# Optimization experiments

Measured on AMD Instinct MI355X. Metric: run time of the kernel, lower is better.

Reference implementation:

```python
import jax, jax.numpy as jnp
import numpy as np

B, T, C, H = 8192, 16, 256, 4
HS = C // H  # 64
FF = 4 * C   # 1024
EPS = 1e-5


def layer_norm(x, g, b):
    mu = jnp.mean(x, axis=-1, keepdims=True)
    var = jnp.var(x, axis=-1, keepdims=True)
    return (x - mu) / jnp.sqrt(var + EPS) * g + b


def setup_inputs() -> dict:
    key = jax.random.key(0)
    ks = jax.random.split(key, 12)
    s = C ** -0.5
    return {
        "x": jax.random.normal(ks[0], (B, T, C), dtype=jnp.float32),
        "Wq": jax.random.normal(ks[1], (H, C, HS), dtype=jnp.float32) * s,
        "Wk": jax.random.normal(ks[2], (H, C, HS), dtype=jnp.float32) * s,
        "Wv": jax.random.normal(ks[3], (H, C, HS), dtype=jnp.float32) * s,
        "Wo": jax.random.normal(ks[4], (C, C), dtype=jnp.float32) * s,
        "bo": jnp.zeros((C,), dtype=jnp.float32),
        "W1": jax.random.normal(ks[5], (C, FF), dtype=jnp.float32) * s,
        "b1": jnp.zeros((FF,), dtype=jnp.float32),
        "W2": jax.random.normal(ks[6], (FF, C), dtype=jnp.float32) * (FF ** -0.5),
        "b2": jnp.zeros((C,), dtype=jnp.float32),
        "g1": jnp.ones((C,), dtype=jnp.float32),
        "be1": jnp.zeros((C,), dtype=jnp.float32),
        "g2": jnp.ones((C,), dtype=jnp.float32),
        "be2": jnp.zeros((C,), dtype=jnp.float32),
    }


def reference(x, Wq, Wk, Wv, Wo, bo, W1, b1, W2, b2, g1, be1, g2, be2):
    # pre-LN attention
    h = layer_norm(x, g1, be1)                       # [B,T,C]
    q = jnp.einsum('btc,hcd->bhtd', h, Wq)
    k = jnp.einsum('btc,hcd->bhtd', h, Wk)
    v = jnp.einsum('btc,hcd->bhtd', h, Wv)
    # NOTE: original scales by n_embed**-0.5 (C), not head_size**-0.5
    scores = jnp.einsum('bhtd,bhsd->bhts', q, k) * (C ** -0.5)
    causal = jnp.tril(jnp.ones((T, T), dtype=bool))
    scores = jnp.where(causal, scores, -jnp.inf)
    w = jax.nn.softmax(scores, axis=-1)
    attn = jnp.einsum('bhts,bhsd->bhtd', w, v)       # [B,H,T,HS]
    attn = attn.transpose(0, 2, 1, 3).reshape(B, T, C)
    x = x + attn @ Wo + bo
    # pre-LN MLP
    h2 = layer_norm(x, g2, be2)
    x = x + jax.nn.relu(h2 @ W1 + b1) @ W2 + b2
    return x
```

## Files before the change

### kernel.cpp

```cpp
#include <hip/hip_runtime.h>
#include <stdint.h>
#include <stddef.h>


#define NTH 512

using f32x4 = __attribute__((ext_vector_type(4))) float;
using s16x8 = __attribute__((ext_vector_type(8))) short;

__device__ __forceinline__ uint16_t f2bf(float f) {
  union { float f; uint32_t u; } v; v.f = f;
  uint32_t r = v.u + 0x7FFF + ((v.u >> 16) & 1);
  return (uint16_t)(r >> 16);
}

__global__ void cvt_qkv(const float* __restrict__ Wq, const float* __restrict__ Wk,
                        const float* __restrict__ Wv, uint16_t* __restrict__ dst) {
  int tid = blockIdx.x * 256 + threadIdx.x;
  if (tid >= 4 * 192 * 256) return;
  int h = tid / (192 * 256);
  int r = tid % (192 * 256);
  int n = r / 256, k = r % 256;
  int comp = n >> 6, d = n & 63;
  const float* src = (comp == 0) ? Wq : ((comp == 1) ? Wk : Wv);
  dst[tid] = f2bf(src[(size_t)h * 256 * 64 + (size_t)k * 64 + d]);
}

__global__ void cvt_t(const float* __restrict__ W, uint16_t* __restrict__ dst,
                      int K, int N) {
  int tid = blockIdx.x * 256 + threadIdx.x;
  if (tid >= K * N) return;
  int n = tid / K, k = tid % K;
  dst[tid] = f2bf(W[(size_t)k * N + n]);
}

#define OFF_H     0
#define OFF_STG   67584
#define OFF_SCR   88064
#define OFF_Q     (OFF_SCR + 0)
#define OFF_K     (OFF_SCR + 18432)
#define OFF_VT    (OFF_SCR + 36864)
#define OFF_P     (OFF_SCR + 61440)
#define OFF_STATS (OFF_SCR + 61440)
#define OFF_U     (OFF_SCR + 0)
#define LDS_BYTES 159744

__device__ __forceinline__ void stageB(const uint16_t* __restrict__ src, int strideK,
                                       int kk0, int nrows, char* stg, int tid) {
  int chunks = nrows * 4;
  for (int idx = tid; idx < chunks; idx += NTH) {
    int n = idx >> 2, o = idx & 3;
    uint4 v = *(const uint4*)(src + (size_t)n * strideK + kk0 + o * 8);
    *(uint4*)(stg + n * 80 + o * 16) = v;
  }
}

__global__ __launch_bounds__(NTH, 2) void block_fused(
    const float* __restrict__ xg,
    const uint16_t* __restrict__ qkvt, const uint16_t* __restrict__ wot,
    const uint16_t* __restrict__ w1t, const uint16_t* __restrict__ w2t,
    const float* __restrict__ bo, const float* __restrict__ b1,
    const float* __restrict__ b2, const float* __restrict__ g1,
    const float* __restrict__ be1, const float* __restrict__ g2,
    const float* __restrict__ be2, float* __restrict__ outg) {
  __shared__ __align__(16) char lds[LDS_BYTES];
  const int tid = threadIdx.x;
  const int wave = tid >> 6, lane = tid & 63;
  const int quad = lane >> 4, l15 = lane & 15;
  const int wr = wave >> 2, wc = wave & 3;
  const int row0 = blockIdx.x * 128;

  {
    uint32_t* z = (uint32_t*)(lds + OFF_VT);
    for (int i = tid; i < (24576 + 10240) / 4; i += NTH) z[i] = 0;
  }

  {
    const int r = tid >> 2;
    const int seg = tid & 3;
    const float* xrow = xg + (size_t)(row0 + r) * 256 + seg * 64;
    float s = 0.f, sq = 0.f;
#pragma unroll
    for (int i = 0; i < 16; ++i) {
      float4 v = ((const float4*)xrow)[i];
      s += v.x + v.y + v.z + v.w;
      sq += v.x * v.x + v.y * v.y + v.z * v.z + v.w * v.w;
    }
    s += __shfl_xor(s, 1); s += __shfl_xor(s, 2);
    sq += __shfl_xor(sq, 1); sq += __shfl_xor(sq, 2);
    float mu = s * (1.f / 256.f);
    float var = sq * (1.f / 256.f) - mu * mu;
    float rstd = rsqrtf(var + 1e-5f);
    char* hrow = lds + OFF_H + r * 528 + seg * 128;
    const float* g1p = g1 + seg * 64;
    const float* e1p = be1 + seg * 64;
#pragma unroll
    for (int i = 0; i < 16; ++i) {
      float4 v = ((const float4*)xrow)[i];
      float4 gv = ((const float4*)g1p)[i];
      float4 bv = ((const float4*)e1p)[i];
      uint32_t p0 = (uint32_t)f2bf((v.x - mu) * rstd * gv.x + bv.x) |
                    ((uint32_t)f2bf((v.y - mu) * rstd * gv.y + bv.y) << 16);
      uint32_t p1 = (uint32_t)f2bf((v.z - mu) * rstd * gv.z + bv.z) |
                    ((uint32_t)f2bf((v.w - mu) * rstd * gv.w + bv.w) << 16);
      uint2 u; u.x = p0; u.y = p1;
      *(uint2*)(hrow + i * 8) = u;
    }
  }
  __syncthreads();

  const f32x4 zero4 = {0.f, 0.f, 0.f, 0.f};
  f32x4 yacc[4][4];
#pragma unroll
  for (int mt = 0; mt < 4; ++mt)
#pragma unroll
    for (int nt = 0; nt < 4; ++nt) yacc[mt][nt] = zero4;

  for (int h = 0; h < 4; ++h) {
    f32x4 qa[4][3];
#pragma unroll
    for (int mt = 0; mt < 4; ++mt)
#pragma unroll
      for (int nt = 0; nt < 3; ++nt) qa[mt][nt] = zero4;
    const uint16_t* wsrc = qkvt + (size_t)h * 192 * 256;
    for (int ks = 0; ks < 8; ++ks) {
      stageB(wsrc, 256, ks * 32, 192, lds + OFF_STG, tid);
      __syncthreads();
      s16x8 af[4], bf[3];
#pragma unroll
      for (int mt = 0; mt < 4; ++mt)
        af[mt] = *(const s16x8*)(lds + OFF_H + (64 * wr + 16 * mt + l15) * 528 +
                                 (ks * 32 + quad * 8) * 2);
#pragma unroll
      for (int nt = 0; nt < 3; ++nt)
        bf[nt] = *(const s16x8*)(lds + OFF_STG + (48 * wc + 16 * nt + l15) * 80 +
                                 quad * 16);
#pragma unroll
      for (int mt = 0; mt < 4; ++mt)
#pragma unroll
        for (int nt = 0; nt < 3; ++nt)
          qa[mt][nt] = __builtin_amdgcn_mfma_f32_16x16x32_bf16(af[mt], bf[nt],
                                                               qa[mt][nt], 0, 0, 0);
      __syncthreads();
    }
#pragma unroll
    for (int mt = 0; mt < 4; ++mt) {
#pragma unroll
      for (int nt = 0; nt < 3; ++nt) {
        int col = 48 * wc + 16 * nt + l15;
        int comp = col >> 6, d = col & 63;
#pragma unroll
        for (int reg = 0; reg < 4; ++reg) {
          int grow = 64 * wr + 16 * mt + 4 * quad + reg;
          uint16_t v = f2bf(qa[mt][nt][reg]);
          if (comp == 0)
            *(uint16_t*)(lds + OFF_Q + grow * 144 + d * 2) = v;
          else if (comp == 1)
            *(uint16_t*)(lds + OFF_K + grow * 144 + d * 2) = v;
          else
            *(uint16_t*)(lds + OFF_VT + (grow >> 4) * 3072 + d * 48 +
                         (grow & 15) * 2) = v;
        }
      }
    }
    __syncthreads();

    {
      f32x4 sacc = zero4;
#pragma unroll
      for (int kk = 0; kk < 2; ++kk) {
        s16x8 aq = *(const s16x8*)(lds + OFF_Q + (16 * wave + l15) * 144 +
                                   (kk * 32 + quad * 8) * 2);
        s16x8 bk = *(const s16x8*)(lds + OFF_K + (16 * wave + l15) * 144 +
                                   (kk * 32 + quad * 8) * 2);
        sacc = __builtin_amdgcn_mfma_f32_16x16x32_bf16(aq, bk, sacc, 0, 0, 0);
      }
      char* pb = lds + OFF_P + wave * 1280;
#pragma unroll
      for (int reg = 0; reg < 4; ++reg) {
        int t = 4 * quad + reg, ss = l15;
        float sc = sacc[reg] * 0.0625f;
        if (ss > t) sc = -1e30f;
        float mx = sc;
#pragma unroll
        for (int d = 1; d < 16; d <<= 1) mx = fmaxf(mx, __shfl_xor(mx, d, 16));
        float e = __expf(sc - mx);
        float sm = e;
#pragma unroll
        for (int d = 1; d < 16; d <<= 1) sm += __shfl_xor(sm, d, 16);
        *(uint16_t*)(pb + t * 80 + ss * 2) = f2bf(e / sm);
      }
      s16x8 ap = *(const s16x8*)(pb + l15 * 80 + quad * 16);
      f32x4 oacc[4];
#pragma unroll
      for (int nt = 0; nt < 4; ++nt) {
        s16x8 bv = *(const s16x8*)(lds + OFF_VT + wave * 3072 +
                                   (16 * nt + l15) * 48 + quad * 16);
        oacc[nt] = __builtin_amdgcn_mfma_f32_16x16x32_bf16(ap, bv, zero4, 0, 0, 0);
      }
#pragma unroll
      for (int nt = 0; nt < 4; ++nt)
#pragma unroll
        for (int reg = 0; reg < 4; ++reg)
          *(uint16_t*)(lds + OFF_Q + (16 * wave + 4 * quad + reg) * 144 +
                       (16 * nt + l15) * 2) = f2bf(oacc[nt][reg]);
    }
    __syncthreads();

    for (int ks = 0; ks < 2; ++ks) {
      stageB(wot, 256, h * 64 + ks * 32, 256, lds + OFF_STG, tid);
      __syncthreads();
      s16x8 af[4], bf[4];
#pragma unroll
      for (int mt = 0; mt < 4; ++mt)
        af[mt] = *(const s16x8*)(lds + OFF_Q + (64 * wr + 16 * mt + l15) * 144 +
                                 (ks * 32 + quad * 8) * 2);
#pragma unroll
      for (int nt = 0; nt < 4; ++nt)
        bf[nt] = *(const s16x8*)(lds + OFF_STG + (64 * wc + 16 * nt + l15) * 80 +
                                 quad * 16);
#pragma unroll
      for (int mt = 0; mt < 4; ++mt)
#pragma unroll
        for (int nt = 0; nt < 4; ++nt)
          yacc[mt][nt] = __builtin_amdgcn_mfma_f32_16x16x32_bf16(af[mt], bf[nt],
                                                                 yacc[mt][nt], 0, 0, 0);
      __syncthreads();
    }
  }

#pragma unroll
  for (int nt = 0; nt < 4; ++nt) {
    int col = 64 * wc + 16 * nt + l15;
    float bov = bo[col];
#pragma unroll
    for (int mt = 0; mt < 4; ++mt)
#pragma unroll
      for (int reg = 0; reg < 4; ++reg) {
        int grow = row0 + 64 * wr + 16 * mt + 4 * quad + reg;
        yacc[mt][nt][reg] += xg[(size_t)grow * 256 + col] + bov;
      }
  }

  {
    float* stats = (float*)(lds + OFF_STATS);
#pragma unroll
    for (int mt = 0; mt < 4; ++mt)
#pragma unroll
      for (int reg = 0; reg < 4; ++reg) {
        float ps = 0.f, pq = 0.f;
#pragma unroll
        for (int nt = 0; nt < 4; ++nt) {
          float v = yacc[mt][nt][reg];
          ps += v; pq += v * v;
        }
#pragma unroll
        for (int d = 1; d < 16; d <<= 1) {
          ps += __shfl_xor(ps, d, 16);
          pq += __shfl_xor(pq, d, 16);
        }
        if (l15 == 0) {
          int lrow = 64 * wr + 16 * mt + 4 * quad + reg;
          stats[lrow * 8 + wc] = ps;
          stats[lrow * 8 + 4 + wc] = pq;
        }
      }
    __syncthreads();
    float g2v[4], e2v[4];
#pragma unroll
    for (int nt = 0; nt < 4; ++nt) {
      int col = 64 * wc + 16 * nt + l15;
      g2v[nt] = g2[col]; e2v[nt] = be2[col];
    }
#pragma unroll
    for (int mt = 0; mt < 4; ++mt)
#pragma unroll
      for (int reg = 0; reg < 4; ++reg) {
        int lrow = 64 * wr + 16 * mt + 4 * quad + reg;
        f32x4 s0 = *(const f32x4*)(stats + lrow * 8);
        f32x4 s1 = *(const f32x4*)(stats + lrow * 8 + 4);
        float mu = (s0[0] + s0[1] + s0[2] + s0[3]) * (1.f / 256.f);
        float var = (s1[0] + s1[1] + s1[2] + s1[3]) * (1.f / 256.f) - mu * mu;
        float rstd = rsqrtf(var + 1e-5f);
#pragma unroll
        for (int nt = 0; nt < 4; ++nt) {
          float hv = (yacc[mt][nt][reg] - mu) * rstd * g2v[nt] + e2v[nt];
          *(uint16_t*)(lds + OFF_H + lrow * 528 + (64 * wc + 16 * nt + l15) * 2) =
              f2bf(hv);
        }
      }
    __syncthreads();
  }

#pragma unroll
  for (int nt = 0; nt < 4; ++nt) {
    float b2v = b2[64 * wc + 16 * nt + l15];
#pragma unroll
    for (int mt = 0; mt < 4; ++mt)
#pragma unroll
      for (int reg = 0; reg < 4; ++reg) yacc[mt][nt][reg] += b2v;
  }
  for (int fc = 0; fc < 4; ++fc) {
    f32x4 ua[4][4];
#pragma unroll
    for (int mt = 0; mt < 4; ++mt)
#pragma unroll
      for (int nt = 0; nt < 4; ++nt) ua[mt][nt] = zero4;
    const uint16_t* w1src = w1t + (size_t)(fc * 256) * 256;
    for (int ks = 0; ks < 8; ++ks) {
      stageB(w1src, 256, ks * 32, 256, lds + OFF_STG, tid);
      __syncthreads();
      s16x8 af[4], bf[4];
#pragma unroll
      for (int mt = 0; mt < 4; ++mt)
        af[mt] = *(const s16x8*)(lds + OFF_H + (64 * wr + 16 * mt + l15) * 528 +
                                 (ks * 32 + quad * 8) * 2);
#pragma unroll
      for (int nt = 0; nt < 4; ++nt)
        bf[nt] = *(const s16x8*)(lds + OFF_STG + (64 * wc + 16 * nt + l15) * 80 +
                                 quad * 16);
#pragma unroll
      for (int mt = 0; mt < 4; ++mt)
#pragma unroll
        for (int nt = 0; nt < 4; ++nt)
          ua[mt][nt] = __builtin_amdgcn_mfma_f32_16x16x32_bf16(af[mt], bf[nt],
                                                               ua[mt][nt], 0, 0, 0);
      __syncthreads();
    }
#pragma unroll
    for (int nt = 0; nt < 4; ++nt) {
      float b1v = b1[fc * 256 + 64 * wc + 16 * nt + l15];
#pragma unroll
      for (int mt = 0; mt < 4; ++mt)
#pragma unroll
        for (int reg = 0; reg < 4; ++reg) {
          float uv = fmaxf(ua[mt][nt][reg] + b1v, 0.f);
          *(uint16_t*)(lds + OFF_U + (64 * wr + 16 * mt + 4 * quad + reg) * 528 +
                       (64 * wc + 16 * nt + l15) * 2) = f2bf(uv);
        }
    }
    __syncthreads();
    for (int ks = 0; ks < 8; ++ks) {
      stageB(w2t, 1024, fc * 256 + ks * 32, 256, lds + OFF_STG, tid);
      __syncthreads();
      s16x8 af[4], bf[4];
#pragma unroll
      for (int mt = 0; mt < 4; ++mt)
        af[mt] = *(const s16x8*)(lds + OFF_U + (64 * wr + 16 * mt + l15) * 528 +
                                 (ks * 32 + quad * 8) * 2);
#pragma unroll
      for (int nt = 0; nt < 4; ++nt)
        bf[nt] = *(const s16x8*)(lds + OFF_STG + (64 * wc + 16 * nt + l15) * 80 +
                                 quad * 16);
#pragma unroll
      for (int mt = 0; mt < 4; ++mt)
#pragma unroll
        for (int nt = 0; nt < 4; ++nt)
          yacc[mt][nt] = __builtin_amdgcn_mfma_f32_16x16x32_bf16(af[mt], bf[nt],
                                                                 yacc[mt][nt], 0, 0, 0);
      __syncthreads();
    }
  }

#pragma unroll
  for (int mt = 0; mt < 4; ++mt)
#pragma unroll
    for (int nt = 0; nt < 4; ++nt) {
      int col = 64 * wc + 16 * nt + l15;
#pragma unroll
      for (int reg = 0; reg < 4; ++reg) {
        int grow = row0 + 64 * wr + 16 * mt + 4 * quad + reg;
        outg[(size_t)grow * 256 + col] = yacc[mt][nt][reg];
      }
    }
}

extern "C" void kernel_launch(void* const* d_in, const int* in_sizes, int n_in,
                              void* d_out, int out_size, void* d_ws, size_t ws_size,
                              hipStream_t stream) {
  (void)in_sizes; (void)n_in; (void)out_size; (void)ws_size;
  const float* x   = (const float*)d_in[0];
  const float* Wq  = (const float*)d_in[1];
  const float* Wk  = (const float*)d_in[2];
  const float* Wv  = (const float*)d_in[3];
  const float* Wo  = (const float*)d_in[4];
  const float* bo  = (const float*)d_in[5];
  const float* W1  = (const float*)d_in[6];
  const float* b1  = (const float*)d_in[7];
  const float* W2  = (const float*)d_in[8];
  const float* b2  = (const float*)d_in[9];
  const float* g1  = (const float*)d_in[10];
  const float* be1 = (const float*)d_in[11];
  const float* g2  = (const float*)d_in[12];
  const float* be2 = (const float*)d_in[13];

  uint16_t* ws   = (uint16_t*)d_ws;
  uint16_t* qkvt = ws;
  uint16_t* wot  = ws + 196608;
  uint16_t* w1t  = ws + 262144;
  uint16_t* w2t  = ws + 524288;

  cvt_qkv<<<768, 256, 0, stream>>>(Wq, Wk, Wv, qkvt);
  cvt_t<<<256, 256, 0, stream>>>(Wo, wot, 256, 256);
  cvt_t<<<1024, 256, 0, stream>>>(W1, w1t, 256, 1024);
  cvt_t<<<1024, 256, 0, stream>>>(W2, w2t, 1024, 256);

  block_fused<<<1024, NTH, 0, stream>>>(x, qkvt, wot, w1t, w2t, bo, b1, b2, g1,
                                        be1, g2, be2, (float*)d_out);
}
```

Measured before the change: 748.5 us.

## Register-prefetch weight tiles in GEMM phases and merge weight conversion kernels

```diff
diff --git a/kernel.cpp b/kernel.cpp
--- a/kernel.cpp
+++ b/kernel.cpp
@@ -14,24 +14,39 @@
   return (uint16_t)(r >> 16);
 }
 
-__global__ void cvt_qkv(const float* __restrict__ Wq, const float* __restrict__ Wk,
-                        const float* __restrict__ Wv, uint16_t* __restrict__ dst) {
-  int tid = blockIdx.x * 256 + threadIdx.x;
-  if (tid >= 4 * 192 * 256) return;
-  int h = tid / (192 * 256);
-  int r = tid % (192 * 256);
-  int n = r / 256, k = r % 256;
-  int comp = n >> 6, d = n & 63;
-  const float* src = (comp == 0) ? Wq : ((comp == 1) ? Wk : Wv);
-  dst[tid] = f2bf(src[(size_t)h * 256 * 64 + (size_t)k * 64 + d]);
-}
-
-__global__ void cvt_t(const float* __restrict__ W, uint16_t* __restrict__ dst,
-                      int K, int N) {
-  int tid = blockIdx.x * 256 + threadIdx.x;
-  if (tid >= K * N) return;
-  int n = tid / K, k = tid % K;
-  dst[tid] = f2bf(W[(size_t)k * N + n]);
+__global__ void cvt_all(const float* __restrict__ Wq, const float* __restrict__ Wk,
+                        const float* __restrict__ Wv, const float* __restrict__ Wo,
+                        const float* __restrict__ W1, const float* __restrict__ W2,
+                        uint16_t* __restrict__ qkvt, uint16_t* __restrict__ wot,
+                        uint16_t* __restrict__ w1t, uint16_t* __restrict__ w2t) {
+  __shared__ float tile[32][33];
+  int b = blockIdx.x;
+  const float* src; uint16_t* dst; int K, N, kt, nt;
+  if (b < 192) {
+    int j = b >> 4, t = b & 15;
+    int h = j / 3, comp = j % 3;
+    src = (comp == 0 ? Wq : (comp == 1 ? Wk : Wv)) + h * 16384;
+    dst = qkvt + h * 192 * 256 + comp * 64 * 256;
+    K = 256; N = 64; kt = t >> 1; nt = t & 1;
+  } else if (b < 256) {
+    int t = b - 192;
+    src = Wo; dst = wot; K = 256; N = 256; kt = t >> 3; nt = t & 7;
+  } else if (b < 512) {
+    int t = b - 256;
+    src = W1; dst = w1t; K = 256; N = 1024; kt = t >> 5; nt = t & 31;
+  } else {
+    int t = b - 512;
+    src = W2; dst = w2t; K = 1024; N = 256; kt = t >> 3; nt = t & 7;
+  }
+  int k0 = kt * 32, n0 = nt * 32;
+  int ty = threadIdx.x >> 5, tx = threadIdx.x & 31;
+#pragma unroll
+  for (int r = 0; r < 4; ++r)
+    tile[ty + 8 * r][tx] = src[(size_t)(k0 + ty + 8 * r) * N + n0 + tx];
+  __syncthreads();
+#pragma unroll
+  for (int r = 0; r < 4; ++r)
+    dst[(size_t)(n0 + ty + 8 * r) * K + k0 + tx] = f2bf(tile[tx][ty + 8 * r]);
 }
 
 #define OFF_H     0
@@ -45,13 +60,51 @@
 #define OFF_U     (OFF_SCR + 0)
 #define LDS_BYTES 159744
 
-__device__ __forceinline__ void stageB(const uint16_t* __restrict__ src, int strideK,
-                                       int kk0, int nrows, char* stg, int tid) {
-  int chunks = nrows * 4;
-  for (int idx = tid; idx < chunks; idx += NTH) {
-    int n = idx >> 2, o = idx & 3;
-    uint4 v = *(const uint4*)(src + (size_t)n * strideK + kk0 + o * 8);
-    *(uint4*)(stg + n * 80 + o * 16) = v;
+template <int NT, int NROWS, int NST>
+__device__ __forceinline__ void gemm_phase(
+    char* lds, const uint16_t* __restrict__ bsrc, int bstrideK,
+    int abase, int astride, f32x4 (&acc)[4][NT],
+    int tid, int wr, int wc, int l15, int quad) {
+  constexpr int CH = NROWS * 4;
+  uint4 pf0, pf1;
+  {
+    int i0 = tid, i1 = tid + NTH;
+    pf0 = *(const uint4*)(bsrc + (size_t)(i0 >> 2) * bstrideK + (i0 & 3) * 8);
+    if (CH > NTH && i1 < CH)
+      pf1 = *(const uint4*)(bsrc + (size_t)(i1 >> 2) * bstrideK + (i1 & 3) * 8);
+  }
+#pragma unroll
+  for (int ks = 0; ks < NST; ++ks) {
+    __syncthreads();
+    {
+      int i0 = tid, i1 = tid + NTH;
+      *(uint4*)(lds + OFF_STG + (i0 >> 2) * 80 + (i0 & 3) * 16) = pf0;
+      if (CH > NTH && i1 < CH)
+        *(uint4*)(lds + OFF_STG + (i1 >> 2) * 80 + (i1 & 3) * 16) = pf1;
+    }
+    __syncthreads();
+    if (ks + 1 < NST) {
+      const uint16_t* bs = bsrc + (ks + 1) * 32;
+      int i0 = tid, i1 = tid + NTH;
+      pf0 = *(const uint4*)(bs + (size_t)(i0 >> 2) * bstrideK + (i0 & 3) * 8);
+      if (CH > NTH && i1 < CH)
+        pf1 = *(const uint4*)(bs + (size_t)(i1 >> 2) * bstrideK + (i1 & 3) * 8);
+    }
+    s16x8 af[4], bfr[NT];
+#pragma unroll
+    for (int mt = 0; mt < 4; ++mt)
+      af[mt] = *(const s16x8*)(lds + abase + (64 * wr + 16 * mt + l15) * astride +
+                               (ks * 32 + quad * 8) * 2);
+#pragma unroll
+    for (int nt = 0; nt < NT; ++nt)
+      bfr[nt] = *(const s16x8*)(lds + OFF_STG +
+                                (NT * 16 * wc + 16 * nt + l15) * 80 + quad * 16);
+#pragma unroll
+    for (int mt = 0; mt < 4; ++mt)
+#pragma unroll
+      for (int nt = 0; nt < NT; ++nt)
+        acc[mt][nt] = __builtin_amdgcn_mfma_f32_16x16x32_bf16(af[mt], bfr[nt],
+                                                              acc[mt][nt], 0, 0, 0);
   }
 }
 
@@ -122,27 +175,8 @@
     for (int mt = 0; mt < 4; ++mt)
 #pragma unroll
       for (int nt = 0; nt < 3; ++nt) qa[mt][nt] = zero4;
-    const uint16_t* wsrc = qkvt + (size_t)h * 192 * 256;
-    for (int ks = 0; ks < 8; ++ks) {
-      stageB(wsrc, 256, ks * 32, 192, lds + OFF_STG, tid);
-      __syncthreads();
-      s16x8 af[4], bf[3];
-#pragma unroll
-      for (int mt = 0; mt < 4; ++mt)
-        af[mt] = *(const s16x8*)(lds + OFF_H + (64 * wr + 16 * mt + l15) * 528 +
-                                 (ks * 32 + quad * 8) * 2);
-#pragma unroll
-      for (int nt = 0; nt < 3; ++nt)
-        bf[nt] = *(const s16x8*)(lds + OFF_STG + (48 * wc + 16 * nt + l15) * 80 +
-                                 quad * 16);
-#pragma unroll
-      for (int mt = 0; mt < 4; ++mt)
-#pragma unroll
-        for (int nt = 0; nt < 3; ++nt)
-          qa[mt][nt] = __builtin_amdgcn_mfma_f32_16x16x32_bf16(af[mt], bf[nt],
-                                                               qa[mt][nt], 0, 0, 0);
-      __syncthreads();
-    }
+    gemm_phase<3, 192, 8>(lds, qkvt + (size_t)h * 192 * 256, 256,
+                          OFF_H, 528, qa, tid, wr, wc, l15, quad);
 #pragma unroll
     for (int mt = 0; mt < 4; ++mt) {
 #pragma unroll
@@ -207,26 +241,9 @@
     }
     __syncthreads();
 
-    for (int ks = 0; ks < 2; ++ks) {
-      stageB(wot, 256, h * 64 + ks * 32, 256, lds + OFF_STG, tid);
-      __syncthreads();
-      s16x8 af[4], bf[4];
-#pragma unroll
-      for (int mt = 0; mt < 4; ++mt)
-        af[mt] = *(const s16x8*)(lds + OFF_Q + (64 * wr + 16 * mt + l15) * 144 +
-                                 (ks * 32 + quad * 8) * 2);
-#pragma unroll
-      for (int nt = 0; nt < 4; ++nt)
-        bf[nt] = *(const s16x8*)(lds + OFF_STG + (64 * wc + 16 * nt + l15) * 80 +
-                                 quad * 16);
-#pragma unroll
-      for (int mt = 0; mt < 4; ++mt)
-#pragma unroll
-        for (int nt = 0; nt < 4; ++nt)
-          yacc[mt][nt] = __builtin_amdgcn_mfma_f32_16x16x32_bf16(af[mt], bf[nt],
-                                                                 yacc[mt][nt], 0, 0, 0);
-      __syncthreads();
-    }
+    gemm_phase<4, 256, 2>(lds, wot + h * 64, 256, OFF_Q, 144, yacc,
+                          tid, wr, wc, l15, quad);
+    __syncthreads();
   }
 
 #pragma unroll
@@ -306,27 +323,9 @@
     for (int mt = 0; mt < 4; ++mt)
 #pragma unroll
       for (int nt = 0; nt < 4; ++nt) ua[mt][nt] = zero4;
-    const uint16_t* w1src = w1t + (size_t)(fc * 256) * 256;
-    for (int ks = 0; ks < 8; ++ks) {
-      stageB(w1src, 256, ks * 32, 256, lds + OFF_STG, tid);
-      __syncthreads();
-      s16x8 af[4], bf[4];
-#pragma unroll
-      for (int mt = 0; mt < 4; ++mt)
-        af[mt] = *(const s16x8*)(lds + OFF_H + (64 * wr + 16 * mt + l15) * 528 +
-                                 (ks * 32 + quad * 8) * 2);
-#pragma unroll
-      for (int nt = 0; nt < 4; ++nt)
-        bf[nt] = *(const s16x8*)(lds + OFF_STG + (64 * wc + 16 * nt + l15) * 80 +
-                                 quad * 16);
-#pragma unroll
-      for (int mt = 0; mt < 4; ++mt)
-#pragma unroll
-        for (int nt = 0; nt < 4; ++nt)
-          ua[mt][nt] = __builtin_amdgcn_mfma_f32_16x16x32_bf16(af[mt], bf[nt],
-                                                               ua[mt][nt], 0, 0, 0);
-      __syncthreads();
-    }
+    gemm_phase<4, 256, 8>(lds, w1t + (size_t)(fc * 256) * 256, 256,
+                          OFF_H, 528, ua, tid, wr, wc, l15, quad);
+    __syncthreads();
 #pragma unroll
     for (int nt = 0; nt < 4; ++nt) {
       float b1v = b1[fc * 256 + 64 * wc + 16 * nt + l15];
@@ -340,26 +339,9 @@
         }
     }
     __syncthreads();
-    for (int ks = 0; ks < 8; ++ks) {
-      stageB(w2t, 1024, fc * 256 + ks * 32, 256, lds + OFF_STG, tid);
-      __syncthreads();
-      s16x8 af[4], bf[4];
-#pragma unroll
-      for (int mt = 0; mt < 4; ++mt)
-        af[mt] = *(const s16x8*)(lds + OFF_U + (64 * wr + 16 * mt + l15) * 528 +
-                                 (ks * 32 + quad * 8) * 2);
-#pragma unroll
-      for (int nt = 0; nt < 4; ++nt)
-        bf[nt] = *(const s16x8*)(lds + OFF_STG + (64 * wc + 16 * nt + l15) * 80 +
-                                 quad * 16);
-#pragma unroll
-      for (int mt = 0; mt < 4; ++mt)
-#pragma unroll
-        for (int nt = 0; nt < 4; ++nt)
-          yacc[mt][nt] = __builtin_amdgcn_mfma_f32_16x16x32_bf16(af[mt], bf[nt],
-                                                                 yacc[mt][nt], 0, 0, 0);
-      __syncthreads();
-    }
+    gemm_phase<4, 256, 8>(lds, w2t + fc * 256, 1024, OFF_U, 528, yacc,
+                          tid, wr, wc, l15, quad);
+    __syncthreads();
   }
 
 #pragma unroll
@@ -400,10 +382,7 @@
   uint16_t* w1t  = ws + 262144;
   uint16_t* w2t  = ws + 524288;
 
-  cvt_qkv<<<768, 256, 0, stream>>>(Wq, Wk, Wv, qkvt);
-  cvt_t<<<256, 256, 0, stream>>>(Wo, wot, 256, 256);
-  cvt_t<<<1024, 256, 0, stream>>>(W1, w1t, 256, 1024);
-  cvt_t<<<1024, 256, 0, stream>>>(W2, w2t, 1024, 256);
+  cvt_all<<<768, 256, 0, stream>>>(Wq, Wk, Wv, Wo, W1, W2, qkvt, wot, w1t, w2t);
 
   block_fused<<<1024, NTH, 0, stream>>>(x, qkvt, wot, w1t, w2t, bo, b1, b2, g1,
                                         be1, g2, be2, (float*)d_out);
```

Result: faster. 638.2 us (-14.7%).
